# Optimization experiments

Hardware: AMD Instinct MI355X
Metric: run time of the kernel (lower is better)

Reference implementation:

```python
import jax, jax.numpy as jnp
import numpy as np

N_NODES = 100000   # adj is [N, N], x is [N, D]
N_EDGES = 625000   # nnz of the COO adjacency
D_FEAT = 128       # embedding dim
EDGE_DROPOUT = 0.1


def setup_inputs() -> dict:
    key = jax.random.key(0)
    k1, k2, k3, k4 = jax.random.split(key, 4)
    x = jax.random.normal(k1, (N_NODES, D_FEAT), dtype=jnp.float32)
    edge_vals = jax.random.uniform(k2, (N_EDGES,), dtype=jnp.float32)
    edge_index = jax.random.randint(k3, (2, N_EDGES), 0, N_NODES)
    # training-mode edge dropout mask: keep edge iff u > edge_dropout
    keep_mask = jax.random.uniform(k4, (N_EDGES,)) > EDGE_DROPOUT
    return {"x": x, "edge_vals": edge_vals, "edge_index": edge_index, "keep_mask": keep_mask}


def reference(x, edge_vals, edge_index, keep_mask):
    # Dropping an edge from the COO tensor == zeroing its value in the SpMM.
    vals = jnp.where(keep_mask, edge_vals, jnp.zeros((), dtype=edge_vals.dtype))
    row = edge_index[0]  # destination rows of adj
    col = edge_index[1]  # source columns of adj
    # out[r] = sum_{e: row[e]==r} vals[e] * x[col[e]]   (torch.sparse.mm(adj, x))
    msgs = vals[:, None] * x[col]                      # [E, D]
    return jax.ops.segment_sum(msgs, row, num_segments=N_NODES)
```

## Files before the change

### kernel.cpp

```cpp
#include <hip/hip_runtime.h>

#define N_NODES 100000
#define N_EDGES 625000
#define D_FEAT  128
#define CAP     32

#define GROUPS      8
#define ROWS_PER_G  (N_NODES / GROUPS)
#define SCAT_BLOCKS ((N_EDGES + 255) / 256)
#define SCAT_TOTAL  (SCAT_BLOCKS * GROUPS)
#define CONV_BLOCKS (N_NODES * D_FEAT / 8 / 256)

#define BF_LO(u) __uint_as_float((u) << 16)
#define BF_HI(u) __uint_as_float((u) & 0xffff0000u)

__device__ __forceinline__ unsigned int rne_bf16(unsigned int u) {
    return (u + 0x7fffu + ((u >> 16) & 1u)) >> 16;
}

__global__ __launch_bounds__(256) void scat_conv(
    const float* __restrict__ x, uint4* __restrict__ xb4,
    const int* __restrict__ ei, const int* __restrict__ keep,
    const float* __restrict__ vals, int* __restrict__ cnt,
    int2* __restrict__ bins)
{
    int b = blockIdx.x;
    if (b < SCAT_TOTAL) {
        int g  = b & 7;
        int e  = (b >> 3) * 256 + threadIdx.x;
        if (e >= N_EDGES) return;
        int r = ei[e];
        if ((unsigned)(r - g * ROWS_PER_G) < (unsigned)ROWS_PER_G && keep[e]) {
            int pos = atomicAdd(&cnt[r], 1);
            if (pos < CAP) {
                int2 pr = { ei[N_EDGES + e], __float_as_int(vals[e]) };
                bins[(long long)r * CAP + pos] = pr;
            }
        }
    } else {
        int i = (b - SCAT_TOTAL) * 256 + threadIdx.x;
        const float4* x4 = reinterpret_cast<const float4*>(x);
        float4 v0 = x4[i * 2], v1 = x4[i * 2 + 1];
        unsigned int a  = rne_bf16(__float_as_uint(v0.x));
        unsigned int bq = rne_bf16(__float_as_uint(v0.y));
        unsigned int c  = rne_bf16(__float_as_uint(v0.z));
        unsigned int d  = rne_bf16(__float_as_uint(v0.w));
        unsigned int e2 = rne_bf16(__float_as_uint(v1.x));
        unsigned int f  = rne_bf16(__float_as_uint(v1.y));
        unsigned int g2 = rne_bf16(__float_as_uint(v1.z));
        unsigned int h  = rne_bf16(__float_as_uint(v1.w));
        uint4 o = { a | (bq << 16), c | (d << 16), e2 | (f << 16), g2 | (h << 16) };
        xb4[i] = o;
    }
}

__global__ __launch_bounds__(256) void gather_bins_bf16(
    const uint4* __restrict__ xb4, const int* __restrict__ cnt,
    const int2* __restrict__ bins, float4* __restrict__ out4)
{
    int gid = blockIdx.x * blockDim.x + threadIdx.x;
    int wave = gid >> 6;
    int lane = threadIdx.x & 63;
    int sub = lane >> 4, l16 = lane & 15;
    int row = wave * 4 + sub;
    if (row >= N_NODES) return;
    int n = cnt[row]; if (n > CAP) n = CAP;
    const int2* bp = bins + (long long)row * CAP;

    float a0=0,a1=0,a2=0,a3=0,a4=0,a5=0,a6=0,a7=0;
    float c0=0,c1=0,c2=0,c3=0,c4=0,c5=0,c6=0,c7=0;
    int p = 0;
    for (; p + 2 <= n; p += 2) {
        int2 e0 = bp[p], e1 = bp[p + 1];
        uint4 g0 = xb4[(long long)e0.x * 16 + l16];
        uint4 g1 = xb4[(long long)e1.x * 16 + l16];
        float v0 = __int_as_float(e0.y), v1 = __int_as_float(e1.y);
        a0 += v0 * BF_LO(g0.x); a1 += v0 * BF_HI(g0.x);
        a2 += v0 * BF_LO(g0.y); a3 += v0 * BF_HI(g0.y);
        a4 += v0 * BF_LO(g0.z); a5 += v0 * BF_HI(g0.z);
        a6 += v0 * BF_LO(g0.w); a7 += v0 * BF_HI(g0.w);
        c0 += v1 * BF_LO(g1.x); c1 += v1 * BF_HI(g1.x);
        c2 += v1 * BF_LO(g1.y); c3 += v1 * BF_HI(g1.y);
        c4 += v1 * BF_LO(g1.z); c5 += v1 * BF_HI(g1.z);
        c6 += v1 * BF_LO(g1.w); c7 += v1 * BF_HI(g1.w);
    }
    if (p < n) {
        int2 e = bp[p];
        uint4 g = xb4[(long long)e.x * 16 + l16];
        float v = __int_as_float(e.y);
        a0 += v * BF_LO(g.x); a1 += v * BF_HI(g.x);
        a2 += v * BF_LO(g.y); a3 += v * BF_HI(g.y);
        a4 += v * BF_LO(g.z); a5 += v * BF_HI(g.z);
        a6 += v * BF_LO(g.w); a7 += v * BF_HI(g.w);
    }
    float4 o0 = { a0 + c0, a1 + c1, a2 + c2, a3 + c3 };
    float4 o1 = { a4 + c4, a5 + c5, a6 + c6, a7 + c7 };
    long long ob = (long long)row * 32 + l16 * 2;
    out4[ob]     = o0;
    out4[ob + 1] = o1;
}

__global__ __launch_bounds__(256) void gather_bins_f32(
    const float* __restrict__ x, const int* __restrict__ cnt,
    const int2* __restrict__ bins, float* __restrict__ out)
{
    int gid = blockIdx.x * blockDim.x + threadIdx.x;
    int row = gid >> 6;
    if (row >= N_NODES) return;
    int lane = threadIdx.x & 63;
    int n = cnt[row]; if (n > CAP) n = CAP;
    const int2* bp = bins + (long long)row * CAP;
    int d = lane * 2;
    float a0 = 0.f, b0 = 0.f, a1 = 0.f, b1 = 0.f;
    int p = 0;
    for (; p + 2 <= n; p += 2) {
        int2 e0 = bp[p], e1 = bp[p + 1];
        float2 x0 = *reinterpret_cast<const float2*>(x + (long long)e0.x * D_FEAT + d);
        float2 x1 = *reinterpret_cast<const float2*>(x + (long long)e1.x * D_FEAT + d);
        float v0 = __int_as_float(e0.y), v1 = __int_as_float(e1.y);
        a0 += v0 * x0.x; b0 += v0 * x0.y;
        a1 += v1 * x1.x; b1 += v1 * x1.y;
    }
    if (p < n) {
        int2 e = bp[p];
        float2 xv = *reinterpret_cast<const float2*>(x + (long long)e.x * D_FEAT + d);
        float v = __int_as_float(e.y);
        a0 += v * xv.x; b0 += v * xv.y;
    }
    float2 o = { a0 + a1, b0 + b1 };
    *reinterpret_cast<float2*>(out + (long long)row * D_FEAT + d) = o;
}

static inline size_t alignup(size_t v) { return (v + 511) / 512 * 512; }

extern "C" void kernel_launch(void* const* d_in, const int* in_sizes, int n_in,
                              void* d_out, int out_size, void* d_ws, size_t ws_size,
                              hipStream_t stream) {
    const float* x    = (const float*)d_in[0];
    const float* vals = (const float*)d_in[1];
    const int*   ei   = (const int*)d_in[2];
    const int*   keep = (const int*)d_in[3];
    float* out = (float*)d_out;

    const size_t sz_xb   = alignup((size_t)N_NODES * D_FEAT * 2);
    const size_t sz_cnt  = alignup((size_t)N_NODES * 4);
    const size_t sz_bins = (size_t)N_NODES * CAP * 8;
    const bool use_bf16 = ws_size >= sz_xb + sz_cnt + sz_bins;

    char* ws = (char*)d_ws;
    uint4* xb4 = nullptr;
    if (use_bf16) { xb4 = (uint4*)ws; ws += sz_xb; }
    int*  cnt  = (int*)ws;  ws += sz_cnt;
    int2* bins = (int2*)ws;

    hipMemsetAsync(cnt, 0, N_NODES * sizeof(int), stream);

    if (use_bf16) {
        scat_conv<<<SCAT_TOTAL + CONV_BLOCKS, 256, 0, stream>>>(
            x, xb4, ei, keep, vals, cnt, bins);
        const long long gthreads = (long long)((N_NODES + 3) / 4) * 64;
        gather_bins_bf16<<<(int)((gthreads + 255) / 256), 256, 0, stream>>>(
            xb4, cnt, bins, (float4*)out);
    } else {
        scat_conv<<<SCAT_TOTAL, 256, 0, stream>>>(
            x, xb4, ei, keep, vals, cnt, bins);
        const long long gthreads = (long long)N_NODES * 64;
        gather_bins_f32<<<(int)((gthreads + 255) / 256), 256, 0, stream>>>(
            x, cnt, bins, out);
    }
}
```

Before: 79.48 us.

## Replace per-row atomic bins with two-pass bucketed CSR build

Drops the per-row fixed-capacity bins filled by global atomics across 8 grouped scatter passes. Edges are now bucketed into 98 coarse row buckets, using shared-memory histograms and one global atomic per bucket per block. A new build_csr kernel then sorts each bucket by local row into a compact CSR segment with row offsets. This cuts global atomic contention and gives the gather contiguous edge lists, at the cost of an extra kernel launch, an extra pass over the edge pairs and a fixed bucket capacity that may overflow.

```diff
diff --git a/kernel.cpp b/kernel.cpp
--- a/kernel.cpp
+++ b/kernel.cpp
@@ -3,12 +3,11 @@
 #define N_NODES 100000
 #define N_EDGES 625000
 #define D_FEAT  128
-#define CAP     32
-
-#define GROUPS      8
-#define ROWS_PER_G  (N_NODES / GROUPS)
-#define SCAT_BLOCKS ((N_EDGES + 255) / 256)
-#define SCAT_TOTAL  (SCAT_BLOCKS * GROUPS)
+
+#define NBKT   98
+#define CAPB   8192
+#define EPB    2048
+#define ABLOCKS ((N_EDGES + EPB - 1) / EPB)
 #define CONV_BLOCKS (N_NODES * D_FEAT / 8 / 256)
 
 #define BF_LO(u) __uint_as_float((u) << 16)
@@ -18,27 +17,50 @@
     return (u + 0x7fffu + ((u >> 16) & 1u)) >> 16;
 }
 
-__global__ __launch_bounds__(256) void scat_conv(
+__global__ __launch_bounds__(256) void bucket_conv(
     const float* __restrict__ x, uint4* __restrict__ xb4,
     const int* __restrict__ ei, const int* __restrict__ keep,
-    const float* __restrict__ vals, int* __restrict__ cnt,
-    int2* __restrict__ bins)
+    const float* __restrict__ vals, int* __restrict__ cursor,
+    int2* __restrict__ pairs)
 {
     int b = blockIdx.x;
-    if (b < SCAT_TOTAL) {
-        int g  = b & 7;
-        int e  = (b >> 3) * 256 + threadIdx.x;
-        if (e >= N_EDGES) return;
-        int r = ei[e];
-        if ((unsigned)(r - g * ROWS_PER_G) < (unsigned)ROWS_PER_G && keep[e]) {
-            int pos = atomicAdd(&cnt[r], 1);
-            if (pos < CAP) {
-                int2 pr = { ei[N_EDGES + e], __float_as_int(vals[e]) };
-                bins[(long long)r * CAP + pos] = pr;
+    if (b < ABLOCKS) {
+        __shared__ int hist[NBKT];
+        __shared__ int run[NBKT];
+        int t = threadIdx.x;
+        for (int i = t; i < NBKT; i += 256) hist[i] = 0;
+        __syncthreads();
+        int base = b * EPB;
+        int   r[8];
+        bool  kp[8];
+        #pragma unroll
+        for (int j = 0; j < 8; ++j) {
+            int e = base + j * 256 + t;
+            bool k = false; int rr = 0;
+            if (e < N_EDGES) { k = (keep[e] != 0); if (k) rr = ei[e]; }
+            kp[j] = k; r[j] = rr;
+            if (k) atomicAdd(&hist[rr >> 10], 1);
+        }
+        __syncthreads();
+        for (int i = t; i < NBKT; i += 256) {
+            int h = hist[i];
+            run[i] = (h > 0) ? atomicAdd(&cursor[i], h) : 0;
+        }
+        __syncthreads();
+        #pragma unroll
+        for (int j = 0; j < 8; ++j) {
+            if (!kp[j]) continue;
+            int e  = base + j * 256 + t;
+            int bk = r[j] >> 10;
+            int pos = atomicAdd(&run[bk], 1);
+            if (pos < CAPB) {
+                int rl = r[j] & 1023;
+                int2 pr = { ei[N_EDGES + e] | (rl << 17), __float_as_int(vals[e]) };
+                pairs[(long long)bk * CAPB + pos] = pr;
             }
         }
     } else {
-        int i = (b - SCAT_TOTAL) * 256 + threadIdx.x;
+        int i = (b - ABLOCKS) * 256 + threadIdx.x;
         const float4* x4 = reinterpret_cast<const float4*>(x);
         float4 v0 = x4[i * 2], v1 = x4[i * 2 + 1];
         unsigned int a  = rne_bf16(__float_as_uint(v0.x));
@@ -54,9 +76,61 @@
     }
 }
 
-__global__ __launch_bounds__(256) void gather_bins_bf16(
-    const uint4* __restrict__ xb4, const int* __restrict__ cnt,
-    const int2* __restrict__ bins, float4* __restrict__ out4)
+__global__ __launch_bounds__(256) void build_csr(
+    const int* __restrict__ cursor, const int2* __restrict__ pairs,
+    int2* __restrict__ fin, int2* __restrict__ rowinfo)
+{
+    __shared__ int hist[1024];
+    __shared__ int ssum[256];
+    int b = blockIdx.x;
+    int t = threadIdx.x;
+    int t4 = t * 4;
+    #pragma unroll
+    for (int i = 0; i < 4; ++i) hist[t4 + i] = 0;
+    __syncthreads();
+    int n = cursor[b]; if (n > CAPB) n = CAPB;
+    const int2* reg = pairs + (long long)b * CAPB;
+    for (int i = t; i < n; i += 256)
+        atomicAdd(&hist[reg[i].x >> 17], 1);
+    __syncthreads();
+    int c0 = hist[t4], c1 = hist[t4 + 1], c2 = hist[t4 + 2], c3 = hist[t4 + 3];
+    ssum[t] = c0 + c1 + c2 + c3;
+    __syncthreads();
+    for (int off = 1; off < 256; off <<= 1) {
+        int add = (t >= off) ? ssum[t - off] : 0;
+        __syncthreads();
+        ssum[t] += add;
+        __syncthreads();
+    }
+    int excl = (t == 0) ? 0 : ssum[t - 1];
+    hist[t4]     = excl;
+    hist[t4 + 1] = excl + c0;
+    hist[t4 + 2] = excl + c0 + c1;
+    hist[t4 + 3] = excl + c0 + c1 + c2;
+    int rbase = b << 10;
+    int gbase = b * CAPB;
+    int cc[4] = { c0, c1, c2, c3 };
+    #pragma unroll
+    for (int i = 0; i < 4; ++i) {
+        int row = rbase + t4 + i;
+        if (row < N_NODES) {
+            int2 ri = { gbase + hist[t4 + i], cc[i] };
+            rowinfo[row] = ri;
+        }
+    }
+    __syncthreads();
+    for (int i = t; i < n; i += 256) {
+        int2 pr = reg[i];
+        int rl = pr.x >> 17;
+        int pos = atomicAdd(&hist[rl], 1);
+        int2 o = { pr.x & 0x1FFFF, pr.y };
+        fin[gbase + pos] = o;
+    }
+}
+
+__global__ __launch_bounds__(256) void gather_csr_bf16(
+    const uint4* __restrict__ xb4, const int2* __restrict__ rowinfo,
+    const int2* __restrict__ fin, float4* __restrict__ out4)
 {
     int gid = blockIdx.x * blockDim.x + threadIdx.x;
     int wave = gid >> 6;
@@ -64,8 +138,9 @@
     int sub = lane >> 4, l16 = lane & 15;
     int row = wave * 4 + sub;
     if (row >= N_NODES) return;
-    int n = cnt[row]; if (n > CAP) n = CAP;
-    const int2* bp = bins + (long long)row * CAP;
+    int2 ri = rowinfo[row];
+    const int2* bp = fin + ri.x;
+    int n = ri.y;
 
     float a0=0,a1=0,a2=0,a3=0,a4=0,a5=0,a6=0,a7=0;
     float c0=0,c1=0,c2=0,c3=0,c4=0,c5=0,c6=0,c7=0;
@@ -100,16 +175,17 @@
     out4[ob + 1] = o1;
 }
 
-__global__ __launch_bounds__(256) void gather_bins_f32(
-    const float* __restrict__ x, const int* __restrict__ cnt,
-    const int2* __restrict__ bins, float* __restrict__ out)
+__global__ __launch_bounds__(256) void gather_csr_f32(
+    const float* __restrict__ x, const int2* __restrict__ rowinfo,
+    const int2* __restrict__ fin, float* __restrict__ out)
 {
     int gid = blockIdx.x * blockDim.x + threadIdx.x;
     int row = gid >> 6;
     if (row >= N_NODES) return;
     int lane = threadIdx.x & 63;
-    int n = cnt[row]; if (n > CAP) n = CAP;
-    const int2* bp = bins + (long long)row * CAP;
+    int2 ri = rowinfo[row];
+    const int2* bp = fin + ri.x;
+    int n = ri.y;
     int d = lane * 2;
     float a0 = 0.f, b0 = 0.f, a1 = 0.f, b1 = 0.f;
     int p = 0;
@@ -143,29 +219,38 @@
     float* out = (float*)d_out;
 
     const size_t sz_xb   = alignup((size_t)N_NODES * D_FEAT * 2);
-    const size_t sz_cnt  = alignup((size_t)N_NODES * 4);
-    const size_t sz_bins = (size_t)N_NODES * CAP * 8;
-    const bool use_bf16 = ws_size >= sz_xb + sz_cnt + sz_bins;
+    const size_t sz_cur  = 512;
+    const size_t sz_pair = (size_t)NBKT * CAPB * 8;
+    const size_t sz_fin  = (size_t)NBKT * CAPB * 8;
+    const size_t sz_ri   = alignup((size_t)N_NODES * 8);
+    const bool use_bf16 = ws_size >= sz_xb + sz_cur + sz_pair + sz_fin + sz_ri;
 
     char* ws = (char*)d_ws;
     uint4* xb4 = nullptr;
     if (use_bf16) { xb4 = (uint4*)ws; ws += sz_xb; }
-    int*  cnt  = (int*)ws;  ws += sz_cnt;
-    int2* bins = (int2*)ws;
-
-    hipMemsetAsync(cnt, 0, N_NODES * sizeof(int), stream);
+    int*  cursor  = (int*)ws;   ws += sz_cur;
+    int2* pairs   = (int2*)ws;  ws += sz_pair;
+    int2* fin     = (int2*)ws;  ws += sz_fin;
+    int2* rowinfo = (int2*)ws;
+
+    hipMemsetAsync(cursor, 0, NBKT * sizeof(int), stream);
 
     if (use_bf16) {
-        scat_conv<<<SCAT_TOTAL + CONV_BLOCKS, 256, 0, stream>>>(
-            x, xb4, ei, keep, vals, cnt, bins);
+        bucket_conv<<<ABLOCKS + CONV_BLOCKS, 256, 0, stream>>>(
+            x, xb4, ei, keep, vals, cursor, pairs);
+    } else {
+        bucket_conv<<<ABLOCKS, 256, 0, stream>>>(
+            x, xb4, ei, keep, vals, cursor, pairs);
+    }
+    build_csr<<<NBKT, 256, 0, stream>>>(cursor, pairs, fin, rowinfo);
+
+    if (use_bf16) {
         const long long gthreads = (long long)((N_NODES + 3) / 4) * 64;
-        gather_bins_bf16<<<(int)((gthreads + 255) / 256), 256, 0, stream>>>(
-            xb4, cnt, bins, (float4*)out);
+        gather_csr_bf16<<<(int)((gthreads + 255) / 256), 256, 0, stream>>>(
+            xb4, rowinfo, fin, (float4*)out);
     } else {
-        scat_conv<<<SCAT_TOTAL, 256, 0, stream>>>(
-            x, xb4, ei, keep, vals, cnt, bins);
         const long long gthreads = (long long)N_NODES * 64;
-        gather_bins_f32<<<(int)((gthreads + 255) / 256), 256, 0, stream>>>(
-            x, cnt, bins, out);
-    }
-}
+        gather_csr_f32<<<(int)((gthreads + 255) / 256), 256, 0, stream>>>(
+            x, rowinfo, fin, out);
+    }
+}
```

Result: no change. 80.96 us (+1.9%).
